# Performance work log

Measured on AMD Instinct MI355X. Metric: run time of the kernel, lower is better.

## Reference

```python
import jax, jax.numpy as jnp
import numpy as np

B, N, T1, T2, K = 16, 2048, 12, 64, 3


def setup_inputs() -> dict:
    key = jax.random.key(0)
    ks = jax.random.split(key, 16)
    g = lambda k, s, sc=1.0: jax.random.normal(k, s, dtype=jnp.float32) * sc
    X = g(ks[0], (B, N, 1, T1))
    A = jax.random.uniform(ks[1], (N, N), dtype=jnp.float32)
    Vs = g(ks[2], (N, N), 1.0 / np.sqrt(N))
    bs = g(ks[3], (N, N), 0.01)
    W1 = jax.random.uniform(ks[4], (T1,), dtype=jnp.float32)
    W2 = g(ks[5], (1, T1), 1.0)
    W3 = jax.random.uniform(ks[6], (1,), dtype=jnp.float32)
    Ve = g(ks[7], (T1, T1), 1.0 / np.sqrt(T1))
    be = g(ks[8], (T1, T1), 0.01)
    U1 = jax.random.uniform(ks[9], (N,), dtype=jnp.float32) / np.sqrt(N)
    U2 = g(ks[10], (1, N), 1.0 / np.sqrt(N))
    U3 = jax.random.uniform(ks[11], (1,), dtype=jnp.float32)
    Wcheb = g(ks[12], (K, T1, T2), 1.0 / np.sqrt(T1))
    bcheb = jnp.zeros((T2,), jnp.float32)
    return dict(X=X, A=A, Vs=Vs, bs=bs, W1=W1, W2=W2, W3=W3, Ve=Ve, be=be,
                U1=U1, U2=U2, U3=U3, Wcheb=Wcheb, bcheb=bcheb)


def reference(X, A, Vs, bs, W1, W2, W3, Ve, be, U1, U2, U3, Wcheb, bcheb):
    # ---- SpatialAtt (C=1). NOTE: faithful to source, the resulting A_hat = A*S
    # is computed in the torch forward but NEVER used downstream (gcn params are
    # built from plain A). jit will DCE this branch.
    W1x = jnp.einsum('bnct,t->bnc', X, W1)            # [B,N,1]
    W3x = jnp.einsum('c,bnct->bnt', W3, X)            # [B,N,T1]
    Ssc = jnp.einsum('bnt,bmt->bnm', jnp.einsum('bnc,ct->bnt', W1x, W2), W3x) + bs
    S = jax.nn.softmax(jnp.einsum('nm,bml->bnl', Vs, jax.nn.softmax(Ssc, axis=1)), axis=1)
    _A_hat = A[None] * S  # unused (matches source)

    # ---- TemporalAtt
    xT = jnp.transpose(X, (0, 3, 2, 1))               # [B,T1,1,N]
    E1 = jnp.einsum('btc,cn->btn', jnp.einsum('btcn,n->btc', xT, U1), U2)  # [B,T1,N]
    U3x = jnp.einsum('c,bnct->bnt', U3, X)            # [B,N,T1]
    Esc = jnp.einsum('btn,bns->bts', E1, U3x) + be    # [B,T1,T1]
    E = jax.nn.softmax(jnp.einsum('ts,bsu->btu', Ve, jax.nn.softmax(Esc, axis=1)), axis=1)

    # E.repeat(1,N,1).view(B,N,T,T) broadcasts the same [T,T] per node
    x2 = X[:, :, 0, :]                                # [B,N,T1]
    X_hat = jnp.einsum('bnt,btu->bnu', x2, E)         # [B,N,T1]

    # ---- ChebConv, sym normalization, lambda_max = 2 -> L_hat = -D^{-1/2} A D^{-1/2}
    # deg from row-sums (scatter over edge_index[0]); aggregation at target (col),
    # so applying L_hat is a transpose-matmul in dense form.
    deg = A.sum(axis=1)
    dis = jnp.where(deg > 0, jax.lax.rsqrt(jnp.where(deg > 0, deg, 1.0)), 0.0)
    M = -(dis[:, None] * A * dis[None, :])            # [N,N]
    Lx = lambda h: jnp.einsum('rc,brt->bct', M, h)    # out[col] += norm * x[row]

    Tx_prev = X_hat
    out = jnp.einsum('bnt,to->bno', X_hat, Wcheb[0])
    Tx = Lx(X_hat)
    if K > 1:
        out = out + jnp.einsum('bnt,to->bno', Tx, Wcheb[1])
    for k in range(2, K):
        Tx_new = 2.0 * Lx(Tx) - Tx_prev
        out = out + jnp.einsum('bnt,to->bno', Tx_new, Wcheb[k])
        Tx_prev, Tx = Tx, Tx_new
    out = jax.nn.relu(out + bcheb)
    return out.reshape(B, N, 1, T2)
```

## Files before the change

kernel.cpp:

```cpp
#include <hip/hip_runtime.h>
#include <math.h>

#define NN 2048
#define BB 16
#define T1D 12
#define T2D 64
#define JJ 192

typedef short short8 __attribute__((ext_vector_type(8)));
typedef float f32x4 __attribute__((ext_vector_type(4)));

#define OFF_DIS   0
#define OFF_E     2048
#define OFF_XH    4608
#define OFF_P1    (OFF_XH + NN*JJ)
#define OFF_XHBT  (OFF_P1 + NN*JJ)
#define OFF_P1BT  (OFF_XHBT + NN*JJ/2)
#define OFF_ABT   (OFF_P1BT + NN*JJ/2)

__device__ inline ushort f2bf(float f) {
    union { float f; unsigned int u; } x; x.f = f;
    unsigned int u = x.u + 0x7fffu + ((x.u >> 16) & 1u);
    return (ushort)(u >> 16);
}

__global__ __launch_bounds__(256) void k_degE(const float* __restrict__ A,
                                              const float* __restrict__ X,
                                              const float* __restrict__ U1,
                                              const float* __restrict__ U2,
                                              const float* __restrict__ U3,
                                              const float* __restrict__ be,
                                              const float* __restrict__ Ve,
                                              float* __restrict__ dis,
                                              float* __restrict__ E_ws) {
    __shared__ float red[24][256];
    __shared__ float es[T1D][T1D];
    int tid = threadIdx.x;

    if (blockIdx.x < 512) {
        int wid = tid >> 6, lane = tid & 63;
        int r = blockIdx.x * 4 + wid;
        const float4* Ar = (const float4*)(A + (size_t)r * NN);
        float s = 0.f;
#pragma unroll
        for (int i = 0; i < 8; ++i) {
            float4 v = Ar[i * 64 + lane];
            s += v.x + v.y + v.z + v.w;
        }
#pragma unroll
        for (int off = 32; off > 0; off >>= 1) s += __shfl_down(s, off);
        if (lane == 0) dis[r] = (s > 0.f) ? rsqrtf(s) : 0.f;
        return;
    }

    int b = blockIdx.x - 512;
    float accr[T1D], accc[T1D];
#pragma unroll
    for (int t = 0; t < T1D; ++t) { accr[t] = 0.f; accc[t] = 0.f; }
    for (int n = tid; n < NN; n += 256) {
        const float* xp = X + ((size_t)b * NN + n) * T1D;
        float x[T1D];
        *(float4*)&x[0] = *(const float4*)&xp[0];
        *(float4*)&x[4] = *(const float4*)&xp[4];
        *(float4*)&x[8] = *(const float4*)&xp[8];
        float u1 = U1[n], u2 = U2[n];
#pragma unroll
        for (int t = 0; t < T1D; ++t) {
            accr[t] += x[t] * u1;
            accc[t] += x[t] * u2;
        }
    }
#pragma unroll
    for (int t = 0; t < T1D; ++t) {
        red[t][tid] = accr[t];
        red[12 + t][tid] = accc[t];
    }
    __syncthreads();
    for (int s = 128; s > 0; s >>= 1) {
        if (tid < s) {
#pragma unroll
            for (int a = 0; a < 24; ++a) red[a][tid] += red[a][tid + s];
        }
        __syncthreads();
    }
    float u3 = U3[0];
    if (tid < T1D) {
        int s = tid;
        float cs = red[12 + s][0] * u3;
        float vals[T1D];
        float m = -1e30f;
#pragma unroll
        for (int t = 0; t < T1D; ++t) {
            vals[t] = red[t][0] * cs + be[t * T1D + s];
            m = fmaxf(m, vals[t]);
        }
        float sum = 0.f;
#pragma unroll
        for (int t = 0; t < T1D; ++t) { vals[t] = expf(vals[t] - m); sum += vals[t]; }
        float inv = 1.f / sum;
#pragma unroll
        for (int t = 0; t < T1D; ++t) es[t][s] = vals[t] * inv;
    }
    __syncthreads();
    if (tid < T1D) {
        int u = tid;
        float vals[T1D];
        float m = -1e30f;
#pragma unroll
        for (int t = 0; t < T1D; ++t) {
            float acc = 0.f;
#pragma unroll
            for (int s = 0; s < T1D; ++s) acc += Ve[t * T1D + s] * es[s][u];
            vals[t] = acc;
            m = fmaxf(m, acc);
        }
        float sum = 0.f;
#pragma unroll
        for (int t = 0; t < T1D; ++t) { vals[t] = expf(vals[t] - m); sum += vals[t]; }
        float inv = 1.f / sum;
#pragma unroll
        for (int t = 0; t < T1D; ++t) E_ws[b * 144 + t * T1D + u] = vals[t] * inv;
    }
}

__global__ __launch_bounds__(256) void k_mid(const float* __restrict__ A,
                                             const float* __restrict__ dis,
                                             const float* __restrict__ X,
                                             const float* __restrict__ E_ws,
                                             ushort* __restrict__ AbT,
                                             float* __restrict__ Xh,
                                             ushort* __restrict__ Xhbt) {
    __shared__ float lds[5504];
    int t = threadIdx.x;

    if (blockIdx.x < 1024) {
        int c0 = (blockIdx.x & 31) * 64, k0 = (blockIdx.x >> 5) * 64;
#pragma unroll
        for (int i = 0; i < 4; ++i) {
            int idx = t + i * 256;
            int kr = idx >> 4, c4 = idx & 15;
            float4 v = *(const float4*)&A[(size_t)(k0 + kr) * NN + c0 + c4 * 4];
            float dk = dis[k0 + kr];
            lds[(c4 * 4 + 0) * 65 + kr] = v.x * dk;
            lds[(c4 * 4 + 1) * 65 + kr] = v.y * dk;
            lds[(c4 * 4 + 2) * 65 + kr] = v.z * dk;
            lds[(c4 * 4 + 3) * 65 + kr] = v.w * dk;
        }
        __syncthreads();
        int cl = t >> 2, ck = (t & 3) * 16;
        float dc = dis[c0 + cl];
        union { ushort us[8]; uint4 v; } p0, p1;
#pragma unroll
        for (int e = 0; e < 8; ++e) p0.us[e] = f2bf(lds[cl * 65 + ck + e] * dc);
#pragma unroll
        for (int e = 0; e < 8; ++e) p1.us[e] = f2bf(lds[cl * 65 + ck + 8 + e] * dc);
        *(uint4*)&AbT[(size_t)(c0 + cl) * NN + k0 + ck] = p0.v;
        *(uint4*)&AbT[(size_t)(c0 + cl) * NN + k0 + ck + 8] = p1.v;
        return;
    }

    int n0 = (blockIdx.x - 1024) * 16;
    float* EL = lds + 3200;
#pragma unroll
    for (int i = 0; i < 9; ++i) {
        int idx = t + i * 256;
        if (idx < 2304) EL[idx] = E_ws[idx];
    }
    __syncthreads();
    {
        int nr = t >> 4, b = t & 15;
        const float* xp = X + ((size_t)b * NN + n0 + nr) * T1D;
        float x[T1D];
        *(float4*)&x[0] = *(const float4*)&xp[0];
        *(float4*)&x[4] = *(const float4*)&xp[4];
        *(float4*)&x[8] = *(const float4*)&xp[8];
        const float* Eb = EL + b * 144;
#pragma unroll
        for (int u = 0; u < T1D; ++u) {
            float acc = 0.f;
#pragma unroll
            for (int tt = 0; tt < T1D; ++tt) acc += x[tt] * Eb[tt * T1D + u];
            lds[nr * 200 + b * T1D + u] = acc;
        }
    }
    __syncthreads();
#pragma unroll
    for (int i = 0; i < 3; ++i) {
        int idx4 = t + i * 256;
        int row = idx4 / 48, c4 = idx4 % 48;
        *(float4*)&Xh[(size_t)(n0 + row) * JJ + c4 * 4] =
            *(float4*)&lds[row * 200 + c4 * 4];
    }
    if (t < JJ) {
        union { ushort us[8]; uint4 v; } p0, p1;
#pragma unroll
        for (int nr = 0; nr < 8; ++nr) p0.us[nr] = f2bf(lds[nr * 200 + t]);
#pragma unroll
        for (int nr = 0; nr < 8; ++nr) p1.us[nr] = f2bf(lds[(8 + nr) * 200 + t]);
        *(uint4*)&Xhbt[(size_t)t * NN + n0] = p0.v;
        *(uint4*)&Xhbt[(size_t)t * NN + n0 + 8] = p1.v;
    }
}

template<int MODE>
__global__ __launch_bounds__(512) void k_gemm(const ushort* __restrict__ AbT,
                                              const ushort* __restrict__ Zbt,
                                              float* __restrict__ P,
                                              ushort* __restrict__ Pbt,
                                              const float* __restrict__ P1,
                                              const float* __restrict__ Xh,
                                              const float* __restrict__ Wcheb,
                                              const float* __restrict__ bcheb,
                                              float* __restrict__ out) {
    __shared__ float lds[8 * 3 * 256 + 16 * 48];
    float* Pred = lds + 6144;
    int tid = threadIdx.x;
    int wave = tid >> 6, lane = tid & 63;
    int jl = lane & 15;
    int kl = (lane >> 4) * 8;
    int c0 = blockIdx.x * 16;
    int j0 = blockIdx.y * 48;
    int kbase = wave * 256 + kl;

    const ushort* arow = AbT + (size_t)(c0 + jl) * NN + kbase;
    f32x4 acc[3];
#pragma unroll
    for (int n = 0; n < 3; ++n) acc[n] = (f32x4)0.f;

#pragma unroll
    for (int ch = 0; ch < 8; ++ch) {
        int koff = ch * 32;
        short8 a = *(const short8*)&arow[koff];
        short8 bfr[3];
#pragma unroll
        for (int n = 0; n < 3; ++n)
            bfr[n] = *(const short8*)&Zbt[(size_t)(j0 + n * 16 + jl) * NN + kbase + koff];
#pragma unroll
        for (int n = 0; n < 3; ++n)
            acc[n] = __builtin_amdgcn_mfma_f32_16x16x32_bf16(a, bfr[n], acc[n], 0, 0, 0);
    }

#pragma unroll
    for (int n = 0; n < 3; ++n)
        *(f32x4*)&lds[((wave * 3 + n) << 8) + (lane << 2)] = acc[n];
    __syncthreads();

    for (int o = tid; o < 768; o += 512) {
        int c_idx = o / 48;
        int j_idx = o - c_idx * 48;
        int n = j_idx >> 4, col = j_idx & 15;
        int lidx = ((c_idx >> 2) * 16 + col) * 4 + (c_idx & 3);
        float s = 0.f;
#pragma unroll
        for (int w = 0; w < 8; ++w) s += lds[(w * 3 + n) * 256 + lidx];
        Pred[c_idx * 48 + j_idx] = s;
        if (MODE == 0) P[(size_t)(c0 + c_idx) * JJ + j0 + j_idx] = s;
    }
    __syncthreads();

    if (MODE == 0) {
        if (tid < 48) {
            union { ushort us[8]; uint4 v; } q0, q1;
#pragma unroll
            for (int e = 0; e < 8; ++e) q0.us[e] = f2bf(Pred[e * 48 + tid]);
#pragma unroll
            for (int e = 0; e < 8; ++e) q1.us[e] = f2bf(Pred[(8 + e) * 48 + tid]);
            *(uint4*)&Pbt[(size_t)(j0 + tid) * NN + c0] = q0.v;
            *(uint4*)&Pbt[(size_t)(j0 + tid) * NN + c0 + 8] = q1.v;
        }
    } else {
        int o = tid & 63, pair = tid >> 6;
        const float* W0 = Wcheb;
        const float* W1 = Wcheb + 768;
        const float* W2 = Wcheb + 1536;
        float w0m2[T1D], w1a[T1D], w2a[T1D];
#pragma unroll
        for (int t = 0; t < T1D; ++t) {
            float w2v = W2[t * 64 + o];
            w0m2[t] = W0[t * 64 + o] - w2v;
            w1a[t] = W1[t * 64 + o];
            w2a[t] = 2.f * w2v;
        }
        float bco = bcheb[o];
#pragma unroll
        for (int it = 0; it < 8; ++it) {
            int pi = pair + it * 8;
            int ni = pi >> 2, bi = pi & 3;
            int n = c0 + ni;
            int b = blockIdx.y * 4 + bi;
            const float* xh = Xh + (size_t)n * JJ + b * T1D;
            const float* p1 = P1 + (size_t)n * JJ + b * T1D;
            const float* p2 = Pred + ni * 48 + bi * T1D;
            float a = bco;
#pragma unroll
            for (int t = 0; t < T1D; ++t)
                a += xh[t] * w0m2[t] - p1[t] * w1a[t] + p2[t] * w2a[t];
            out[(size_t)((b << 11) + n) * 64 + o] = fmaxf(a, 0.f);
        }
    }
}

extern "C" void kernel_launch(void* const* d_in, const int* in_sizes, int n_in,
                              void* d_out, int out_size, void* d_ws, size_t ws_size,
                              hipStream_t stream) {
    const float* X  = (const float*)d_in[0];
    const float* A  = (const float*)d_in[1];
    const float* Ve = (const float*)d_in[7];
    const float* be = (const float*)d_in[8];
    const float* U1 = (const float*)d_in[9];
    const float* U2 = (const float*)d_in[10];
    const float* U3 = (const float*)d_in[11];
    const float* Wc = (const float*)d_in[12];
    const float* bc = (const float*)d_in[13];
    float* out = (float*)d_out;

    float* w     = (float*)d_ws;
    float* dis   = w + OFF_DIS;
    float* E     = w + OFF_E;
    float* Xh    = w + OFF_XH;
    float* P1    = w + OFF_P1;
    ushort* Xhbt = (ushort*)(w + OFF_XHBT);
    ushort* P1bt = (ushort*)(w + OFF_P1BT);
    ushort* AbT  = (ushort*)(w + OFF_ABT);

    k_degE<<<528, 256, 0, stream>>>(A, X, U1, U2, U3, be, Ve, dis, E);
    k_mid<<<1152, 256, 0, stream>>>(A, dis, X, E, AbT, Xh, Xhbt);
    k_gemm<0><<<dim3(128, 4), 512, 0, stream>>>(AbT, Xhbt, P1, P1bt,
                                                nullptr, nullptr, nullptr, nullptr, nullptr);
    k_gemm<1><<<dim3(128, 4), 512, 0, stream>>>(AbT, P1bt, nullptr, nullptr,
                                                P1, Xh, Wc, bc, out);
}
```

Baseline: 168.9 us.

## Fuse all stages into one cooperative persistent kernel with grid syncs

Replaces the four separate launches (degree/temporal attention, matrix prep, two GEMMs) with a single cooperative kernel of 256 blocks that runs each stage in turn and separates them with grid-wide syncs. Each block loops over several tiles per stage. The aim is to remove launch overhead and inter-kernel gaps. In exchange, grid.sync has its own cost, per-stage parallelism is lower (256 blocks of 512 threads), and the old launch path remains as a fallback if the cooperative launch fails.

```diff
diff --git a/kernel.cpp b/kernel.cpp
--- a/kernel.cpp
+++ b/kernel.cpp
@@ -1,5 +1,8 @@
 #include <hip/hip_runtime.h>
+#include <hip/hip_cooperative_groups.h>
 #include <math.h>
+
+namespace cg = cooperative_groups;
 
 #define NN 2048
 #define BB 16
@@ -22,6 +25,299 @@
     union { float f; unsigned int u; } x; x.f = f;
     unsigned int u = x.u + 0x7fffu + ((x.u >> 16) & 1u);
     return (ushort)(u >> 16);
+}
+
+template<int MODE>
+__device__ __forceinline__ void gemm_body(int blk2, int tid, float* lds,
+                                          const ushort* __restrict__ AbT,
+                                          const ushort* __restrict__ Zbt,
+                                          float* __restrict__ P,
+                                          ushort* __restrict__ Pbt,
+                                          const float* __restrict__ P1,
+                                          const float* __restrict__ Xh,
+                                          const float* __restrict__ Wcheb,
+                                          const float* __restrict__ bcheb,
+                                          float* __restrict__ out) {
+    float* Pred = lds + 6144;
+    int wave = tid >> 6, lane = tid & 63;
+    int jl = lane & 15;
+    int kl = (lane >> 4) * 8;
+    int c0 = (blk2 >> 2) * 16;
+    int j0 = (blk2 & 3) * 48;
+    int kbase = wave * 256 + kl;
+
+    const ushort* arow = AbT + (size_t)(c0 + jl) * NN + kbase;
+    f32x4 acc[3];
+#pragma unroll
+    for (int n = 0; n < 3; ++n) acc[n] = (f32x4)0.f;
+
+#pragma unroll
+    for (int ch = 0; ch < 8; ++ch) {
+        int koff = ch * 32;
+        short8 a = *(const short8*)&arow[koff];
+        short8 bfr[3];
+#pragma unroll
+        for (int n = 0; n < 3; ++n)
+            bfr[n] = *(const short8*)&Zbt[(size_t)(j0 + n * 16 + jl) * NN + kbase + koff];
+#pragma unroll
+        for (int n = 0; n < 3; ++n)
+            acc[n] = __builtin_amdgcn_mfma_f32_16x16x32_bf16(a, bfr[n], acc[n], 0, 0, 0);
+    }
+
+#pragma unroll
+    for (int n = 0; n < 3; ++n)
+        *(f32x4*)&lds[((wave * 3 + n) << 8) + (lane << 2)] = acc[n];
+    __syncthreads();
+
+    for (int o = tid; o < 768; o += 512) {
+        int c_idx = o / 48;
+        int j_idx = o - c_idx * 48;
+        int n = j_idx >> 4, col = j_idx & 15;
+        int lidx = ((c_idx >> 2) * 16 + col) * 4 + (c_idx & 3);
+        float s = 0.f;
+#pragma unroll
+        for (int w = 0; w < 8; ++w) s += lds[(w * 3 + n) * 256 + lidx];
+        Pred[c_idx * 48 + j_idx] = s;
+        if (MODE == 0) P[(size_t)(c0 + c_idx) * JJ + j0 + j_idx] = s;
+    }
+    __syncthreads();
+
+    if (MODE == 0) {
+        if (tid < 48) {
+            union { ushort us[8]; uint4 v; } q0, q1;
+#pragma unroll
+            for (int e = 0; e < 8; ++e) q0.us[e] = f2bf(Pred[e * 48 + tid]);
+#pragma unroll
+            for (int e = 0; e < 8; ++e) q1.us[e] = f2bf(Pred[(8 + e) * 48 + tid]);
+            *(uint4*)&Pbt[(size_t)(j0 + tid) * NN + c0] = q0.v;
+            *(uint4*)&Pbt[(size_t)(j0 + tid) * NN + c0 + 8] = q1.v;
+        }
+    } else {
+        int o = tid & 63, pair = tid >> 6;
+        const float* W0 = Wcheb;
+        const float* W1 = Wcheb + 768;
+        const float* W2 = Wcheb + 1536;
+        float w0m2[T1D], w1a[T1D], w2a[T1D];
+#pragma unroll
+        for (int t = 0; t < T1D; ++t) {
+            float w2v = W2[t * 64 + o];
+            w0m2[t] = W0[t * 64 + o] - w2v;
+            w1a[t] = W1[t * 64 + o];
+            w2a[t] = 2.f * w2v;
+        }
+        float bco = bcheb[o];
+#pragma unroll
+        for (int it = 0; it < 8; ++it) {
+            int pi = pair + it * 8;
+            int ni = pi >> 2, bi = pi & 3;
+            int n = c0 + ni;
+            int b = (blk2 & 3) * 4 + bi;
+            const float* xh = Xh + (size_t)n * JJ + b * T1D;
+            const float* p1 = P1 + (size_t)n * JJ + b * T1D;
+            const float* p2 = Pred + ni * 48 + bi * T1D;
+            float a = bco;
+#pragma unroll
+            for (int t = 0; t < T1D; ++t)
+                a += xh[t] * w0m2[t] - p1[t] * w1a[t] + p2[t] * w2a[t];
+            out[(size_t)((b << 11) + n) * 64 + o] = fmaxf(a, 0.f);
+        }
+    }
+}
+
+__global__ __launch_bounds__(512, 2) void k_mega(
+        const float* __restrict__ A, const float* __restrict__ X,
+        const float* __restrict__ U1, const float* __restrict__ U2,
+        const float* __restrict__ U3, const float* __restrict__ be,
+        const float* __restrict__ Ve, const float* __restrict__ Wc,
+        const float* __restrict__ bc,
+        float* __restrict__ dis, float* __restrict__ E_ws,
+        float* __restrict__ Xh, float* __restrict__ P1,
+        ushort* __restrict__ Xhbt, ushort* __restrict__ P1bt,
+        ushort* __restrict__ AbT, float* __restrict__ out) {
+    cg::grid_group grid = cg::this_grid();
+    __shared__ float lds[6912];
+    int tid = threadIdx.x;
+    int blk = blockIdx.x;
+
+    {
+        int wave = tid >> 6, lane = tid & 63;
+        int r = blk * 8 + wave;
+        const float4* Ar = (const float4*)(A + (size_t)r * NN);
+        float s = 0.f;
+#pragma unroll
+        for (int i = 0; i < 8; ++i) {
+            float4 v = Ar[i * 64 + lane];
+            s += v.x + v.y + v.z + v.w;
+        }
+#pragma unroll
+        for (int off = 32; off > 0; off >>= 1) s += __shfl_down(s, off);
+        if (lane == 0) dis[r] = (s > 0.f) ? rsqrtf(s) : 0.f;
+    }
+    if (blk < 16) {
+        int b = blk;
+        float accr[T1D], accc[T1D];
+#pragma unroll
+        for (int t = 0; t < T1D; ++t) { accr[t] = 0.f; accc[t] = 0.f; }
+        for (int n = tid; n < NN; n += 512) {
+            const float* xp = X + ((size_t)b * NN + n) * T1D;
+            float x[T1D];
+            *(float4*)&x[0] = *(const float4*)&xp[0];
+            *(float4*)&x[4] = *(const float4*)&xp[4];
+            *(float4*)&x[8] = *(const float4*)&xp[8];
+            float u1 = U1[n], u2 = U2[n];
+#pragma unroll
+            for (int t = 0; t < T1D; ++t) {
+                accr[t] += x[t] * u1;
+                accc[t] += x[t] * u2;
+            }
+        }
+#pragma unroll
+        for (int off = 32; off > 0; off >>= 1) {
+#pragma unroll
+            for (int t = 0; t < T1D; ++t) {
+                accr[t] += __shfl_down(accr[t], off);
+                accc[t] += __shfl_down(accc[t], off);
+            }
+        }
+        float* red24  = lds;
+        float* es     = lds + 192;
+        float* redtot = lds + 352;
+        int wave = tid >> 6, lane = tid & 63;
+        if (lane == 0) {
+#pragma unroll
+            for (int t = 0; t < T1D; ++t) {
+                red24[t * 8 + wave] = accr[t];
+                red24[(12 + t) * 8 + wave] = accc[t];
+            }
+        }
+        __syncthreads();
+        if (tid < 24) {
+            float s = 0.f;
+#pragma unroll
+            for (int w = 0; w < 8; ++w) s += red24[tid * 8 + w];
+            redtot[tid] = s;
+        }
+        __syncthreads();
+        float u3 = U3[0];
+        if (tid < T1D) {
+            int s = tid;
+            float cs = redtot[12 + s] * u3;
+            float vals[T1D];
+            float m = -1e30f;
+#pragma unroll
+            for (int t = 0; t < T1D; ++t) {
+                vals[t] = redtot[t] * cs + be[t * T1D + s];
+                m = fmaxf(m, vals[t]);
+            }
+            float sum = 0.f;
+#pragma unroll
+            for (int t = 0; t < T1D; ++t) { vals[t] = expf(vals[t] - m); sum += vals[t]; }
+            float inv = 1.f / sum;
+#pragma unroll
+            for (int t = 0; t < T1D; ++t) es[t * T1D + s] = vals[t] * inv;
+        }
+        __syncthreads();
+        if (tid < T1D) {
+            int u = tid;
+            float vals[T1D];
+            float m = -1e30f;
+#pragma unroll
+            for (int t = 0; t < T1D; ++t) {
+                float acc = 0.f;
+#pragma unroll
+                for (int s = 0; s < T1D; ++s) acc += Ve[t * T1D + s] * es[s * T1D + u];
+                vals[t] = acc;
+                m = fmaxf(m, acc);
+            }
+            float sum = 0.f;
+#pragma unroll
+            for (int t = 0; t < T1D; ++t) { vals[t] = expf(vals[t] - m); sum += vals[t]; }
+            float inv = 1.f / sum;
+#pragma unroll
+            for (int t = 0; t < T1D; ++t) E_ws[b * 144 + t * T1D + u] = vals[t] * inv;
+        }
+    }
+    grid.sync();
+
+#pragma unroll 1
+    for (int tt = 0; tt < 4; ++tt) {
+        int tile = blk * 4 + tt;
+        int c0 = (tile & 31) * 64, k0 = (tile >> 5) * 64;
+        __syncthreads();
+#pragma unroll
+        for (int i = 0; i < 2; ++i) {
+            int idx = tid + i * 512;
+            int kr = idx >> 4, c4 = idx & 15;
+            float4 v = *(const float4*)&A[(size_t)(k0 + kr) * NN + c0 + c4 * 4];
+            float dk = dis[k0 + kr];
+            lds[(c4 * 4 + 0) * 65 + kr] = v.x * dk;
+            lds[(c4 * 4 + 1) * 65 + kr] = v.y * dk;
+            lds[(c4 * 4 + 2) * 65 + kr] = v.z * dk;
+            lds[(c4 * 4 + 3) * 65 + kr] = v.w * dk;
+        }
+        __syncthreads();
+        int cl = tid >> 3, ck = (tid & 7) * 8;
+        float dc = dis[c0 + cl];
+        union { ushort us[8]; uint4 v; } p;
+#pragma unroll
+        for (int e = 0; e < 8; ++e) p.us[e] = f2bf(lds[cl * 65 + ck + e] * dc);
+        *(uint4*)&AbT[(size_t)(c0 + cl) * NN + k0 + ck] = p.v;
+    }
+    {
+        __syncthreads();
+        int n0 = blk * 8;
+        float* EL = lds + 4352;
+#pragma unroll
+        for (int i = 0; i < 5; ++i) {
+            int idx = tid + i * 512;
+            if (idx < 2304) EL[idx] = E_ws[idx];
+        }
+        __syncthreads();
+        if (tid < 128) {
+            int nr = tid >> 4, b = tid & 15;
+            const float* xp = X + ((size_t)b * NN + n0 + nr) * T1D;
+            float x[T1D];
+            *(float4*)&x[0] = *(const float4*)&xp[0];
+            *(float4*)&x[4] = *(const float4*)&xp[4];
+            *(float4*)&x[8] = *(const float4*)&xp[8];
+            const float* Eb = EL + b * 144;
+#pragma unroll
+            for (int u = 0; u < T1D; ++u) {
+                float acc = 0.f;
+#pragma unroll
+                for (int t2 = 0; t2 < T1D; ++t2) acc += x[t2] * Eb[t2 * T1D + u];
+                lds[nr * 200 + b * T1D + u] = acc;
+            }
+        }
+        __syncthreads();
+        if (tid < 384) {
+            int row = tid / 48, c4 = tid % 48;
+            *(float4*)&Xh[(size_t)(n0 + row) * JJ + c4 * 4] =
+                *(float4*)&lds[row * 200 + c4 * 4];
+        }
+        if (tid < JJ) {
+            union { ushort us[8]; uint4 v; } p0;
+#pragma unroll
+            for (int nr = 0; nr < 8; ++nr) p0.us[nr] = f2bf(lds[nr * 200 + tid]);
+            *(uint4*)&Xhbt[(size_t)tid * NN + n0] = p0.v;
+        }
+    }
+    grid.sync();
+
+#pragma unroll 1
+    for (int s = 0; s < 2; ++s) {
+        __syncthreads();
+        gemm_body<0>(blk * 2 + s, tid, lds, AbT, Xhbt, P1, P1bt,
+                     nullptr, nullptr, nullptr, nullptr, nullptr);
+    }
+    grid.sync();
+
+#pragma unroll 1
+    for (int s = 0; s < 2; ++s) {
+        __syncthreads();
+        gemm_body<1>(blk * 2 + s, tid, lds, AbT, P1bt, nullptr, nullptr,
+                     P1, Xh, Wc, bc, out);
+    }
 }
 
 __global__ __launch_bounds__(256) void k_degE(const float* __restrict__ A,
@@ -213,91 +509,9 @@
                                               const float* __restrict__ bcheb,
                                               float* __restrict__ out) {
     __shared__ float lds[8 * 3 * 256 + 16 * 48];
-    float* Pred = lds + 6144;
-    int tid = threadIdx.x;
-    int wave = tid >> 6, lane = tid & 63;
-    int jl = lane & 15;
-    int kl = (lane >> 4) * 8;
-    int c0 = blockIdx.x * 16;
-    int j0 = blockIdx.y * 48;
-    int kbase = wave * 256 + kl;
-
-    const ushort* arow = AbT + (size_t)(c0 + jl) * NN + kbase;
-    f32x4 acc[3];
-#pragma unroll
-    for (int n = 0; n < 3; ++n) acc[n] = (f32x4)0.f;
-
-#pragma unroll
-    for (int ch = 0; ch < 8; ++ch) {
-        int koff = ch * 32;
-        short8 a = *(const short8*)&arow[koff];
-        short8 bfr[3];
-#pragma unroll
-        for (int n = 0; n < 3; ++n)
-            bfr[n] = *(const short8*)&Zbt[(size_t)(j0 + n * 16 + jl) * NN + kbase + koff];
-#pragma unroll
-        for (int n = 0; n < 3; ++n)
-            acc[n] = __builtin_amdgcn_mfma_f32_16x16x32_bf16(a, bfr[n], acc[n], 0, 0, 0);
-    }
-
-#pragma unroll
-    for (int n = 0; n < 3; ++n)
-        *(f32x4*)&lds[((wave * 3 + n) << 8) + (lane << 2)] = acc[n];
-    __syncthreads();
-
-    for (int o = tid; o < 768; o += 512) {
-        int c_idx = o / 48;
-        int j_idx = o - c_idx * 48;
-        int n = j_idx >> 4, col = j_idx & 15;
-        int lidx = ((c_idx >> 2) * 16 + col) * 4 + (c_idx & 3);
-        float s = 0.f;
-#pragma unroll
-        for (int w = 0; w < 8; ++w) s += lds[(w * 3 + n) * 256 + lidx];
-        Pred[c_idx * 48 + j_idx] = s;
-        if (MODE == 0) P[(size_t)(c0 + c_idx) * JJ + j0 + j_idx] = s;
-    }
-    __syncthreads();
-
-    if (MODE == 0) {
-        if (tid < 48) {
-            union { ushort us[8]; uint4 v; } q0, q1;
-#pragma unroll
-            for (int e = 0; e < 8; ++e) q0.us[e] = f2bf(Pred[e * 48 + tid]);
-#pragma unroll
-            for (int e = 0; e < 8; ++e) q1.us[e] = f2bf(Pred[(8 + e) * 48 + tid]);
-            *(uint4*)&Pbt[(size_t)(j0 + tid) * NN + c0] = q0.v;
-            *(uint4*)&Pbt[(size_t)(j0 + tid) * NN + c0 + 8] = q1.v;
-        }
-    } else {
-        int o = tid & 63, pair = tid >> 6;
-        const float* W0 = Wcheb;
-        const float* W1 = Wcheb + 768;
-        const float* W2 = Wcheb + 1536;
-        float w0m2[T1D], w1a[T1D], w2a[T1D];
-#pragma unroll
-        for (int t = 0; t < T1D; ++t) {
-            float w2v = W2[t * 64 + o];
-            w0m2[t] = W0[t * 64 + o] - w2v;
-            w1a[t] = W1[t * 64 + o];
-            w2a[t] = 2.f * w2v;
-        }
-        float bco = bcheb[o];
-#pragma unroll
-        for (int it = 0; it < 8; ++it) {
-            int pi = pair + it * 8;
-            int ni = pi >> 2, bi = pi & 3;
-            int n = c0 + ni;
-            int b = blockIdx.y * 4 + bi;
-            const float* xh = Xh + (size_t)n * JJ + b * T1D;
-            const float* p1 = P1 + (size_t)n * JJ + b * T1D;
-            const float* p2 = Pred + ni * 48 + bi * T1D;
-            float a = bco;
-#pragma unroll
-            for (int t = 0; t < T1D; ++t)
-                a += xh[t] * w0m2[t] - p1[t] * w1a[t] + p2[t] * w2a[t];
-            out[(size_t)((b << 11) + n) * 64 + o] = fmaxf(a, 0.f);
-        }
-    }
+    int blk2 = blockIdx.x * 4 + blockIdx.y;
+    gemm_body<MODE>(blk2, threadIdx.x, lds, AbT, Zbt, P, Pbt,
+                    P1, Xh, Wcheb, bcheb, out);
 }
 
 extern "C" void kernel_launch(void* const* d_in, const int* in_sizes, int n_in,
@@ -323,10 +537,19 @@
     ushort* P1bt = (ushort*)(w + OFF_P1BT);
     ushort* AbT  = (ushort*)(w + OFF_ABT);
 
-    k_degE<<<528, 256, 0, stream>>>(A, X, U1, U2, U3, be, Ve, dis, E);
-    k_mid<<<1152, 256, 0, stream>>>(A, dis, X, E, AbT, Xh, Xhbt);
-    k_gemm<0><<<dim3(128, 4), 512, 0, stream>>>(AbT, Xhbt, P1, P1bt,
-                                                nullptr, nullptr, nullptr, nullptr, nullptr);
-    k_gemm<1><<<dim3(128, 4), 512, 0, stream>>>(AbT, P1bt, nullptr, nullptr,
-                                                P1, Xh, Wc, bc, out);
-}
+    void* args[] = { (void*)&A, (void*)&X, (void*)&U1, (void*)&U2, (void*)&U3,
+                     (void*)&be, (void*)&Ve, (void*)&Wc, (void*)&bc,
+                     (void*)&dis, (void*)&E, (void*)&Xh, (void*)&P1,
+                     (void*)&Xhbt, (void*)&P1bt, (void*)&AbT, (void*)&out };
+    hipError_t err = hipLaunchCooperativeKernel((const void*)k_mega, dim3(256),
+                                                dim3(512), args, 0, stream);
+    if (err != hipSuccess) {
+        k_degE<<<528, 256, 0, stream>>>(A, X, U1, U2, U3, be, Ve, dis, E);
+        k_mid<<<1152, 256, 0, stream>>>(A, dis, X, E, AbT, Xh, Xhbt);
+        k_gemm<0><<<dim3(128, 4), 512, 0, stream>>>(AbT, Xhbt, P1, P1bt,
+                                                    nullptr, nullptr, nullptr,
+                                                    nullptr, nullptr);
+        k_gemm<1><<<dim3(128, 4), 512, 0, stream>>>(AbT, P1bt, nullptr, nullptr,
+                                                    P1, Xh, Wc, bc, out);
+    }
+}
```

Result: slower. 274.5 us (+62.5%).
